# Kernel optimization log

Measured on AMD Instinct MI355X. Metric: run time of the kernel, lower is better.

The kernel has to match this reference:

```python
import jax, jax.numpy as jnp
import numpy as np

B, E, H, NY, NX = 16, 128, 4, 32, 32


def setup_inputs() -> dict:
    key = jax.random.key(0)
    ks = jax.random.split(key, 7)
    w = lambda k, shape: jax.random.normal(k, shape, jnp.float32) * 0.02
    return {
        "x": jax.random.normal(ks[0], (B, E, NY, NX), jnp.float32),
        "Wk": w(ks[1], (E, E)), "bk": jnp.zeros((E,), jnp.float32),
        "Wq": w(ks[2], (E, E)), "bq": jnp.zeros((E,), jnp.float32),
        "Wv": w(ks[3], (E, E)), "bv": jnp.zeros((E,), jnp.float32),
        "Wu": w(ks[4], (E, E)), "bu": jnp.zeros((E,), jnp.float32),
        "pos_enc": w(ks[5], (H, (2 * NY - 1) * (2 * NX - 1))),
    }


def _conv1x1(x, W, b):
    # 1x1 conv == channel-mixing linear: (B,C,y,x) -> (B,O,y,x)
    return jnp.einsum('bcyx,oc->boyx', x, W) + b[None, :, None, None]


def _rel_indices(ny, nx):
    y = jnp.arange(ny)
    x = jnp.arange(nx)
    y1, x1, y2, x2 = jnp.meshgrid(y, x, y, x, indexing='ij')
    idx = (y1 - y2 + ny - 1) * (2 * nx - 1) + (x1 - x2 + nx - 1)
    return idx.reshape(ny * nx, ny * nx)  # (N, N)


def reference(x, Wk, bk, Wq, bq, Wv, bv, Wu, bu, pos_enc):
    b, e, ny, nx = x.shape
    h = pos_enc.shape[0]
    hc = e // h
    n = ny * nx
    scale = hc ** (-0.5)

    keys = _conv1x1(x, Wk, bk).reshape(b, h, hc, n)
    queries = _conv1x1(x, Wq, bq).reshape(b, h, hc, n)
    values = _conv1x1(x, Wv, bv).reshape(b, h, hc, n)

    # att[b,h,k,q] = sum_c keys[b,h,c,k] * queries[b,h,c,q]
    att = jnp.einsum('bhck,bhcq->bhkq', keys, queries) * scale

    # gathered relative position bias: (H, N, N)
    idx = _rel_indices(ny, nx)
    rel = pos_enc[:, idx]
    att = att + rel[None]

    # softmax over the key axis (dim=-2), as in the original
    att = jax.nn.softmax(att, axis=-2)

    out = jnp.einsum('bhck,bhkq->bhcq', values, att).reshape(b, e, ny, nx)
    return _conv1x1(out, Wu, bu)
```

## Files before the change

kernel.cpp:

```cpp
#include <hip/hip_runtime.h>
#include <hip/hip_bf16.h>

#define BN 16
#define EN 128
#define HN 4
#define HCN 32
#define NN 1024
#define POSN 3969

typedef short short8 __attribute__((ext_vector_type(8)));
typedef float f32x4 __attribute__((ext_vector_type(4)));

#define MFMA16(a, b, c) __builtin_amdgcn_mfma_f32_16x16x32_bf16((a), (b), (c), 0, 0, 0)

union Frag {
  short8 s8;
  uint2 u2[2];
  unsigned int u[4];
  unsigned short us[8];
};

__device__ __forceinline__ unsigned short bfbits(float x) {
  union { __hip_bfloat16 h; unsigned short u; } c;
  c.h = __float2bfloat16(x);
  return c.u;
}

__device__ __forceinline__ unsigned int pk2(float lo, float hi) {
  union { __hip_bfloat162 h2; unsigned int u; } c;
  c.h2 = __float22bfloat162_rn(make_float2(lo, hi));
  return c.u;
}

__global__ __launch_bounds__(256) void prep_kernel(
    const float* __restrict__ pos,
    const float* __restrict__ Wk, const float* __restrict__ Wq,
    const float* __restrict__ Wv, const float* __restrict__ Wu,
    unsigned short* __restrict__ bias, Frag* __restrict__ wtab,
    Frag* __restrict__ whitab, Frag* __restrict__ wlotab)
{
  const int b0 = blockIdx.x, t = threadIdx.x;
  if (b0 < 189) {
    const int gid = b0 * 256 + t;
    const int l = gid & 63;
    const int t2 = gid >> 6;
    const int dxi = t2 % 3;
    const int dy31 = (t2 / 3) % 63;
    const int h = t2 / 189;
    const int rowk0 = (l >> 4) * 4, colq = l & 15;
    const float log2e = 1.4426950408889634f;
    unsigned int bits[4];
#pragma unroll
    for (int j = 0; j < 4; ++j) {
      const int dx = (dxi - 1) * 16 + rowk0 + j - colq + 31;
      bits[j] = (unsigned int)bfbits(pos[h * POSN + dy31 * 63 + dx] * log2e);
    }
    uint2 o;
    o.x = bits[0] | (bits[1] << 16);
    o.y = bits[2] | (bits[3] << 16);
    *(uint2*)(bias + (size_t)gid * 4) = o;
  } else if (b0 < 213) {
    const int fid = (b0 - 189) * 256 + t;
    const int z = fid >> 11, rem = fid & 2047;
    const int ot = rem >> 8, ks = (rem >> 6) & 3, l = rem & 63;
    const float* W = (z == 0) ? Wk : (z == 1) ? Wq : Wv;
    const int o = ot * 16 + (l & 15), lq = l >> 4;
    const float* wp = W + (size_t)o * EN + ks * 32 + lq * 4;
    float4 wa = *(const float4*)wp;
    float4 wb2 = *(const float4*)(wp + 16);
    Frag f;
    f.u[0] = pk2(wa.x, wa.y);   f.u[1] = pk2(wa.z, wa.w);
    f.u[2] = pk2(wb2.x, wb2.y); f.u[3] = pk2(wb2.z, wb2.w);
    wtab[fid] = f;
  } else {
    const int fid = (b0 - 213) * 256 + t;
    const int ot = fid >> 8, ks = (fid >> 6) & 3, l = fid & 63;
    const int o = ot * 16 + (l & 15), lq = l >> 4;
    const float* wp = Wu + (size_t)o * EN + ks * 32 + lq * 4;
    float4 wa = *(const float4*)wp;
    float4 wb2 = *(const float4*)(wp + 16);
    float v[8] = {wa.x, wa.y, wa.z, wa.w, wb2.x, wb2.y, wb2.z, wb2.w};
    unsigned short hb[8]; float lf[8];
#pragma unroll
    for (int e = 0; e < 8; ++e) {
      __hip_bfloat16 hh = __float2bfloat16(v[e]);
      union { __hip_bfloat16 h; unsigned short u; } c; c.h = hh;
      hb[e] = c.u;
      lf[e] = v[e] - __bfloat162float(hh);
    }
    Frag fh, fl;
#pragma unroll
    for (int e = 0; e < 4; ++e)
      fh.u[e] = hb[2 * e] | ((unsigned int)hb[2 * e + 1] << 16);
    fl.u[0] = pk2(lf[0], lf[1]); fl.u[1] = pk2(lf[2], lf[3]);
    fl.u[2] = pk2(lf[4], lf[5]); fl.u[3] = pk2(lf[6], lf[7]);
    whitab[fid] = fh;
    wlotab[fid] = fl;
  }
}

__global__ __launch_bounds__(256) void conv_qkv_mfma(
    const float* __restrict__ x, const Frag* __restrict__ wtab,
    const float* __restrict__ bk, __hip_bfloat16* __restrict__ kb,
    const float* __restrict__ bq, __hip_bfloat16* __restrict__ qb,
    const float* __restrict__ bv, __hip_bfloat16* __restrict__ vb)
{
  const int n0 = blockIdx.x * 32;
  const int bb = blockIdx.y;
  const int t = threadIdx.x, w = t >> 6, l = t & 63;
  const int l15 = l & 15, lq = l >> 4;

  __shared__ unsigned short xs[32][132];

  {
    const float* xb = x + (size_t)bb * EN * NN + n0;
    const int n = t & 31, cg = (t >> 5) * 4;
#pragma unroll
    for (int i = 0; i < 4; ++i) {
      const int cb = cg + i * 32;
      float a0 = xb[(size_t)(cb + 0) * NN + n];
      float a1 = xb[(size_t)(cb + 1) * NN + n];
      float a2 = xb[(size_t)(cb + 2) * NN + n];
      float a3 = xb[(size_t)(cb + 3) * NN + n];
      uint2 v; v.x = pk2(a0, a1); v.y = pk2(a2, a3);
      *(uint2*)&xs[n][cb] = v;
    }
  }
  __syncthreads();

#pragma unroll
  for (int z = 0; z < 3; ++z) {
    const float* bias = (z == 0) ? bk : (z == 1) ? bq : bv;
    __hip_bfloat16* out = (z == 0) ? kb : (z == 1) ? qb : vb;

    Frag wf[2][4];
#pragma unroll
    for (int r = 0; r < 2; ++r)
#pragma unroll
      for (int ks = 0; ks < 4; ++ks)
        wf[r][ks] = wtab[(((size_t)z * 8 + (w * 2 + r)) * 4 + ks) * 64 + l];

    f32x4 acc[2][2];
#pragma unroll
    for (int r = 0; r < 2; ++r)
#pragma unroll
      for (int nt = 0; nt < 2; ++nt) acc[r][nt] = 0.f;

#pragma unroll
    for (int ks = 0; ks < 4; ++ks) {
#pragma unroll
      for (int nt = 0; nt < 2; ++nt) {
        Frag xf;
        xf.u2[0] = *(const uint2*)&xs[nt * 16 + l15][ks * 32 + lq * 4];
        xf.u2[1] = *(const uint2*)&xs[nt * 16 + l15][ks * 32 + lq * 4 + 16];
        if (z < 2) {
          acc[0][nt] = MFMA16(wf[0][ks].s8, xf.s8, acc[0][nt]);
          acc[1][nt] = MFMA16(wf[1][ks].s8, xf.s8, acc[1][nt]);
        } else {
          acc[0][nt] = MFMA16(xf.s8, wf[0][ks].s8, acc[0][nt]);
          acc[1][nt] = MFMA16(xf.s8, wf[1][ks].s8, acc[1][nt]);
        }
      }
    }

    if (z < 2) {
#pragma unroll
      for (int r = 0; r < 2; ++r) {
        const int ob = (w * 2 + r) * 16 + lq * 4;
        const int hh = ob >> 5;
        const int pofs = hh * 32 + ((ob >> 2) & 3) * 8 + ((ob & 16) ? 4 : 0);
        float4 b4 = *(const float4*)(bias + ob);
#pragma unroll
        for (int nt = 0; nt < 2; ++nt) {
          const int n = n0 + nt * 16 + l15;
          f32x4 a = acc[r][nt];
          uint2 o2;
          o2.x = pk2(a[0] + b4.x, a[1] + b4.y);
          o2.y = pk2(a[2] + b4.z, a[3] + b4.w);
          *(uint2*)(out + (size_t)(bb * NN + n) * 128 + pofs) = o2;
        }
      }
    } else {
#pragma unroll
      for (int r = 0; r < 2; ++r) {
        const int o = (w * 2 + r) * 16 + l15;
        const int c = o & 31, hh = o >> 5;
        const float bsc = bias[o];
#pragma unroll
        for (int nt = 0; nt < 2; ++nt) {
          const int nb = n0 + nt * 16 + lq * 4;
          const int kbk = nb >> 5, k32 = nb & 31;
          const int pofs = ((k32 >> 2) & 3) * 8 + ((k32 & 16) ? 4 : 0);
          f32x4 a = acc[r][nt];
          uint2 o2;
          o2.x = pk2(a[0] + bsc, a[1] + bsc);
          o2.y = pk2(a[2] + bsc, a[3] + bsc);
          *(uint2*)(out + ((size_t)((bb * 4 + hh) * 32 + c) * 32 + kbk) * 32 + pofs) = o2;
        }
      }
    }
  }
}

__global__ __launch_bounds__(256, 4) void attn_mfma_kernel(
    const __hip_bfloat16* __restrict__ kp,
    const __hip_bfloat16* __restrict__ qp,
    const __hip_bfloat16* __restrict__ vp,
    const unsigned short* __restrict__ bias,
    __hip_bfloat16* __restrict__ Opb,
    float* __restrict__ lp)
{
  const int bx = blockIdx.x;
  const int qi = bx & 7, s = bx >> 3;
  const int h = blockIdx.y, b = blockIdx.z;
  const int t = threadIdx.x, w = t >> 6, l = t & 63;
  const int l15 = l & 15, lq = l >> 4;

  __shared__ Frag Kf[2][8][64];
  __shared__ Frag Vf[2][8][64];

  const __hip_bfloat16* kBase = kp + (size_t)b * 131072 + h * 32 + (size_t)l15 * 128 + lq * 8;
  const __hip_bfloat16* vBase = vp + (size_t)((b * 4 + h) * 32 + l15) * 1024 + lq * 8;
  const unsigned short* biasB = bias + (size_t)h * 48384 + l * 4;

#define KADDR(CHG, KT) ((const Frag*)(kBase + (size_t)((CHG) * 128 + (KT) * 16) * 128))
#define VADDR(CHG, SL) ((const Frag*)(vBase + (size_t)((SL) >> 2) * 16384 + ((CHG) * 4 + ((SL) & 3)) * 32))

  const int qt0 = qi * 8 + w * 2;
  Frag qf[2];
  qf[0] = *(const Frag*)(qp + (size_t)(b * 1024 + (qt0 + 0) * 16 + l15) * 128 + h * 32 + lq * 8);
  qf[1] = *(const Frag*)(qp + (size_t)(b * 1024 + (qt0 + 1) * 16 + l15) * 128 + h * 32 + lq * 8);
  const int qy[2] = {(qt0 + 0) >> 1, (qt0 + 1) >> 1};
  const int qx1[2] = {(qt0 + 0) & 1, (qt0 + 1) & 1};

  {
    const int chg = s * 4;
    Kf[0][w][l]     = *KADDR(chg, w);
    Kf[0][w + 4][l] = *KADDR(chg, w + 4);
    Vf[0][w][l]     = *VADDR(chg, w);
    Vf[0][w + 4][l] = *VADDR(chg, w + 4);
  }
  __syncthreads();

  f32x4 O[2][2];
#pragma unroll
  for (int mt = 0; mt < 2; ++mt)
#pragma unroll
    for (int nt = 0; nt < 2; ++nt) O[mt][nt] = 0.f;
  f32x4 Lacc[2]; Lacc[0] = 0.f; Lacc[1] = 0.f;

  Frag ones;
  ones.u[0] = 0x3F803F80u; ones.u[1] = 0x3F803F80u;
  ones.u[2] = 0x3F803F80u; ones.u[3] = 0x3F803F80u;

  const float SCALE2 = 0.17677669529663687f * 1.4426950408889634f;

  for (int c4 = 0; c4 < 4; ++c4) {
    const int buf = c4 & 1;
    const int chg = s * 4 + c4;

    Frag kn[2], vn[2];
    if (c4 < 3) {
      kn[0] = *KADDR(chg + 1, w);
      kn[1] = *KADDR(chg + 1, w + 4);
      vn[0] = *VADDR(chg + 1, w);
      vn[1] = *VADDR(chg + 1, w + 4);
    }

#pragma unroll
    for (int hh2 = 0; hh2 < 2; ++hh2) {
      short8 ka[4], va[4];
#pragma unroll
      for (int kt = 0; kt < 4; ++kt) ka[kt] = Kf[buf][hh2 * 4 + kt][l].s8;
#pragma unroll
      for (int mt = 0; mt < 2; ++mt)
#pragma unroll
        for (int kh = 0; kh < 2; ++kh)
          va[mt * 2 + kh] = Vf[buf][mt * 4 + hh2 * 2 + kh][l].s8;

#pragma unroll
      for (int nt = 0; nt < 2; ++nt) {
        uint2 bw[4];
#pragma unroll
        for (int kt = 0; kt < 4; ++kt) {
          const int ktg = chg * 8 + hh2 * 4 + kt;
          const int off = ((ktg >> 1) - qy[nt] + 31) * 768 + ((ktg & 1) - qx1[nt] + 1) * 256;
          bw[kt] = *(const uint2*)(biasB + off);
        }

        __builtin_amdgcn_s_setprio(1);
        f32x4 S[4];
#pragma unroll
        for (int kt = 0; kt < 4; ++kt) {
          f32x4 z = 0.f;
          S[kt] = MFMA16(ka[kt], qf[nt].s8, z);
        }
        __builtin_amdgcn_s_setprio(0);

        Frag B0, B1;
#pragma unroll
        for (int kt = 0; kt < 4; ++kt) {
          const float b0 = __uint_as_float(bw[kt].x << 16);
          const float b1 = __uint_as_float(bw[kt].x & 0xffff0000u);
          const float b2 = __uint_as_float(bw[kt].y << 16);
          const float b3 = __uint_as_float(bw[kt].y & 0xffff0000u);
          float p0 = exp2f(fmaf(S[kt][0], SCALE2, b0));
          float p1 = exp2f(fmaf(S[kt][1], SCALE2, b1));
          float p2 = exp2f(fmaf(S[kt][2], SCALE2, b2));
          float p3 = exp2f(fmaf(S[kt][3], SCALE2, b3));
          unsigned int lo = pk2(p0, p1), hi = pk2(p2, p3);
          if (kt < 2) { B0.u[kt * 2] = lo; B0.u[kt * 2 + 1] = hi; }
          else        { B1.u[(kt - 2) * 2] = lo; B1.u[(kt - 2) * 2 + 1] = hi; }
        }

        __builtin_amdgcn_s_setprio(1);
        O[0][nt] = MFMA16(va[0], B0.s8, O[0][nt]);
        O[0][nt] = MFMA16(va[1], B1.s8, O[0][nt]);
        O[1][nt] = MFMA16(va[2], B0.s8, O[1][nt]);
        O[1][nt] = MFMA16(va[3], B1.s8, O[1][nt]);
        Lacc[nt] = MFMA16(ones.s8, B0.s8, Lacc[nt]);
        Lacc[nt] = MFMA16(ones.s8, B1.s8, Lacc[nt]);
        __builtin_amdgcn_s_setprio(0);
      }
    }

    if (c4 < 3) {
      Kf[buf ^ 1][w][l]     = kn[0];
      Kf[buf ^ 1][w + 4][l] = kn[1];
      Vf[buf ^ 1][w][l]     = vn[0];
      Vf[buf ^ 1][w + 4][l] = vn[1];
      __syncthreads();
    }
  }
#undef KADDR
#undef VADDR

  if (lq == 0) {
#pragma unroll
    for (int nt = 0; nt < 2; ++nt)
      lp[((size_t)(s * 16 + b) * 4 + h) * 1024 + (qt0 + nt) * 16 + l15] = Lacc[nt][0];
  }

  __hip_bfloat16* obb = Opb + ((size_t)(s * 16 + b) * 1024) * 128 + h * 32 + lq * 8;
#pragma unroll
  for (int nt = 0; nt < 2; ++nt) {
    const int n = (qt0 + nt) * 16 + l15;
    Frag f;
    f.u[0] = pk2(O[0][nt][0], O[0][nt][1]);
    f.u[1] = pk2(O[0][nt][2], O[0][nt][3]);
    f.u[2] = pk2(O[1][nt][0], O[1][nt][1]);
    f.u[3] = pk2(O[1][nt][2], O[1][nt][3]);
    *(Frag*)(obb + (size_t)n * 128) = f;
  }
}

__global__ __launch_bounds__(256, 2) void conv_final_mfma(
    const __hip_bfloat16* __restrict__ Opb,
    const float* __restrict__ lp,
    const Frag* __restrict__ whitab, const Frag* __restrict__ wlotab,
    const float* __restrict__ bu, float* __restrict__ out)
{
  const int n0 = blockIdx.x * 32;
  const int bb = blockIdx.y;
  const int t = threadIdx.x, w = t >> 6, l = t & 63;
  const int l15 = l & 15, lq = l >> 4;

  __shared__ float rls[4][32];
  if (t < 128) {
    const int h = t >> 5, nl = t & 31;
    const float l0 = lp[((size_t)(0 * 16 + bb) * 4 + h) * 1024 + n0 + nl];
    const float l1 = lp[((size_t)(1 * 16 + bb) * 4 + h) * 1024 + n0 + nl];
    rls[h][nl] = 1.0f / (l0 + l1);
  }

  Frag whi[2][4], wlo[2][4];
#pragma unroll
  for (int r = 0; r < 2; ++r)
#pragma unroll
    for (int ks = 0; ks < 4; ++ks) {
      const int idx = (((w * 2 + r) * 4) + ks) * 64 + l;
      whi[r][ks] = whitab[idx];
      wlo[r][ks] = wlotab[idx];
    }
  __syncthreads();

  f32x4 acc[2][2];
#pragma unroll
  for (int r = 0; r < 2; ++r)
#pragma unroll
    for (int nt = 0; nt < 2; ++nt) acc[r][nt] = 0.f;

#pragma unroll
  for (int s = 0; s < 2; ++s) {
#pragma unroll
    for (int h = 0; h < 4; ++h) {
      Frag a2[2];
#pragma unroll
      for (int nt = 0; nt < 2; ++nt) {
        const int n = n0 + nt * 16 + l15;
        Frag af = *(const Frag*)(Opb + ((size_t)((s * 16 + bb) * 1024 + n)) * 128 + h * 32 + lq * 8);
        const float sc = rls[h][nt * 16 + l15];
        Frag as;
#pragma unroll
        for (int e = 0; e < 4; ++e) {
          const float f0 = __uint_as_float((unsigned int)af.us[2 * e] << 16) * sc;
          const float f1 = __uint_as_float((unsigned int)af.us[2 * e + 1] << 16) * sc;
          as.u[e] = pk2(f0, f1);
        }
        a2[nt] = as;
      }
#pragma unroll
      for (int r = 0; r < 2; ++r)
#pragma unroll
        for (int nt = 0; nt < 2; ++nt) {
          acc[r][nt] = MFMA16(a2[nt].s8, whi[r][h].s8, acc[r][nt]);
          acc[r][nt] = MFMA16(a2[nt].s8, wlo[r][h].s8, acc[r][nt]);
        }
    }
  }

#pragma unroll
  for (int r = 0; r < 2; ++r) {
    const int o = (w * 2 + r) * 16 + l15;
    const float bo = bu[o];
#pragma unroll
    for (int nt = 0; nt < 2; ++nt) {
      const int nb = n0 + nt * 16 + lq * 4;
      f32x4 a = acc[r][nt];
      float4 res = make_float4(a[0] + bo, a[1] + bo, a[2] + bo, a[3] + bo);
      *(float4*)(out + ((size_t)bb * EN + o) * NN + nb) = res;
    }
  }
}

extern "C" void kernel_launch(void* const* d_in, const int* in_sizes, int n_in,
                              void* d_out, int out_size, void* d_ws, size_t ws_size,
                              hipStream_t stream)
{
  const float* x   = (const float*)d_in[0];
  const float* Wk  = (const float*)d_in[1];
  const float* bk  = (const float*)d_in[2];
  const float* Wq  = (const float*)d_in[3];
  const float* bq  = (const float*)d_in[4];
  const float* Wv  = (const float*)d_in[5];
  const float* bv  = (const float*)d_in[6];
  const float* Wu  = (const float*)d_in[7];
  const float* bu  = (const float*)d_in[8];
  const float* pos = (const float*)d_in[9];

  char* ws = (char*)d_ws;
  __hip_bfloat16* kb = (__hip_bfloat16*)(ws);
  __hip_bfloat16* qb = (__hip_bfloat16*)(ws + (size_t)4194304);
  __hip_bfloat16* vb = (__hip_bfloat16*)(ws + (size_t)8388608);
  unsigned short* bias = (unsigned short*)(ws + (size_t)12582912);
  Frag* wtab   = (Frag*)(ws + (size_t)12969984);
  Frag* whitab = (Frag*)(ws + (size_t)13068288);
  Frag* wlotab = (Frag*)(ws + (size_t)13101056);
  float* lp = (float*)(ws + (size_t)13133824);
  __hip_bfloat16* Opb = (__hip_bfloat16*)(ws + (size_t)13658112);

  prep_kernel<<<221, 256, 0, stream>>>(pos, Wk, Wq, Wv, Wu, bias, wtab, whitab, wlotab);

  dim3 g1(32, BN);
  conv_qkv_mfma<<<g1, 256, 0, stream>>>(x, wtab, bk, kb, bq, qb, bv, vb);

  dim3 g2(16, HN, BN);
  attn_mfma_kernel<<<g2, 256, 0, stream>>>(kb, qb, vb, bias, Opb, lp);

  dim3 g3(32, BN);
  conv_final_mfma<<<g3, 256, 0, stream>>>(Opb, lp, whitab, wlotab, bu, (float*)d_out);
}
```

Before: 59.30 us.

## Merge prep and QKV conv kernels; use direct global-to-LDS loads in attention

Folds the prep kernel (bias table and Wu hi/lo split) into the QKV conv kernel as extra blocks. The conv blocks now read and convert Wk/Wq/Wv to bf16 fragments themselves, so the wtab table and one kernel launch go away. In attention, K/V double-buffer prefetch uses global_load_lds, which writes straight into LDS instead of going through registers. All bias loads for a chunk are also hoisted ahead of compute. In exchange, the conv blocks do redundant weight conversion, and register pressure from the hoisted bias array rises.

New measurement: 66.76 us. +12.6%, slower.

```diff
diff --git a/kernel.cpp b/kernel.cpp
--- a/kernel.cpp
+++ b/kernel.cpp
@@ -32,82 +32,73 @@
   return c.u;
 }
 
-__global__ __launch_bounds__(256) void prep_kernel(
-    const float* __restrict__ pos,
-    const float* __restrict__ Wk, const float* __restrict__ Wq,
-    const float* __restrict__ Wv, const float* __restrict__ Wu,
-    unsigned short* __restrict__ bias, Frag* __restrict__ wtab,
-    Frag* __restrict__ whitab, Frag* __restrict__ wlotab)
+__device__ __forceinline__ void load_lds16(const void* g, void* l) {
+  __builtin_amdgcn_global_load_lds(
+      (const __attribute__((address_space(1))) void*)g,
+      (__attribute__((address_space(3))) void*)l, 16, 0, 0);
+}
+
+__global__ __launch_bounds__(256) void qkv_prep_kernel(
+    const float* __restrict__ x,
+    const float* __restrict__ Wk, const float* __restrict__ bk, __hip_bfloat16* __restrict__ kb,
+    const float* __restrict__ Wq, const float* __restrict__ bq, __hip_bfloat16* __restrict__ qb,
+    const float* __restrict__ Wv, const float* __restrict__ bv, __hip_bfloat16* __restrict__ vb,
+    const float* __restrict__ Wu, const float* __restrict__ pos,
+    unsigned short* __restrict__ bias, Frag* __restrict__ whitab, Frag* __restrict__ wlotab)
 {
-  const int b0 = blockIdx.x, t = threadIdx.x;
-  if (b0 < 189) {
-    const int gid = b0 * 256 + t;
-    const int l = gid & 63;
-    const int t2 = gid >> 6;
-    const int dxi = t2 % 3;
-    const int dy31 = (t2 / 3) % 63;
-    const int h = t2 / 189;
-    const int rowk0 = (l >> 4) * 4, colq = l & 15;
-    const float log2e = 1.4426950408889634f;
-    unsigned int bits[4];
-#pragma unroll
-    for (int j = 0; j < 4; ++j) {
-      const int dx = (dxi - 1) * 16 + rowk0 + j - colq + 31;
-      bits[j] = (unsigned int)bfbits(pos[h * POSN + dy31 * 63 + dx] * log2e);
-    }
-    uint2 o;
-    o.x = bits[0] | (bits[1] << 16);
-    o.y = bits[2] | (bits[3] << 16);
-    *(uint2*)(bias + (size_t)gid * 4) = o;
-  } else if (b0 < 213) {
-    const int fid = (b0 - 189) * 256 + t;
-    const int z = fid >> 11, rem = fid & 2047;
-    const int ot = rem >> 8, ks = (rem >> 6) & 3, l = rem & 63;
-    const float* W = (z == 0) ? Wk : (z == 1) ? Wq : Wv;
-    const int o = ot * 16 + (l & 15), lq = l >> 4;
-    const float* wp = W + (size_t)o * EN + ks * 32 + lq * 4;
-    float4 wa = *(const float4*)wp;
-    float4 wb2 = *(const float4*)(wp + 16);
-    Frag f;
-    f.u[0] = pk2(wa.x, wa.y);   f.u[1] = pk2(wa.z, wa.w);
-    f.u[2] = pk2(wb2.x, wb2.y); f.u[3] = pk2(wb2.z, wb2.w);
-    wtab[fid] = f;
-  } else {
-    const int fid = (b0 - 213) * 256 + t;
-    const int ot = fid >> 8, ks = (fid >> 6) & 3, l = fid & 63;
-    const int o = ot * 16 + (l & 15), lq = l >> 4;
-    const float* wp = Wu + (size_t)o * EN + ks * 32 + lq * 4;
-    float4 wa = *(const float4*)wp;
-    float4 wb2 = *(const float4*)(wp + 16);
-    float v[8] = {wa.x, wa.y, wa.z, wa.w, wb2.x, wb2.y, wb2.z, wb2.w};
-    unsigned short hb[8]; float lf[8];
-#pragma unroll
-    for (int e = 0; e < 8; ++e) {
-      __hip_bfloat16 hh = __float2bfloat16(v[e]);
-      union { __hip_bfloat16 h; unsigned short u; } c; c.h = hh;
-      hb[e] = c.u;
-      lf[e] = v[e] - __bfloat162float(hh);
-    }
-    Frag fh, fl;
-#pragma unroll
-    for (int e = 0; e < 4; ++e)
-      fh.u[e] = hb[2 * e] | ((unsigned int)hb[2 * e + 1] << 16);
-    fl.u[0] = pk2(lf[0], lf[1]); fl.u[1] = pk2(lf[2], lf[3]);
-    fl.u[2] = pk2(lf[4], lf[5]); fl.u[3] = pk2(lf[6], lf[7]);
-    whitab[fid] = fh;
-    wlotab[fid] = fl;
-  }
-}
-
-__global__ __launch_bounds__(256) void conv_qkv_mfma(
-    const float* __restrict__ x, const Frag* __restrict__ wtab,
-    const float* __restrict__ bk, __hip_bfloat16* __restrict__ kb,
-    const float* __restrict__ bq, __hip_bfloat16* __restrict__ qb,
-    const float* __restrict__ bv, __hip_bfloat16* __restrict__ vb)
-{
-  const int n0 = blockIdx.x * 32;
-  const int bb = blockIdx.y;
-  const int t = threadIdx.x, w = t >> 6, l = t & 63;
+  const int bid = blockIdx.x, t = threadIdx.x;
+
+  if (bid >= 512) {
+    if (bid < 701) {
+      const int gid = (bid - 512) * 256 + t;
+      const int l = gid & 63;
+      const int t2 = gid >> 6;
+      const int dxi = t2 % 3;
+      const int dy31 = (t2 / 3) % 63;
+      const int h = t2 / 189;
+      const int rowk0 = (l >> 4) * 4, colq = l & 15;
+      const float log2e = 1.4426950408889634f;
+      unsigned int bits[4];
+#pragma unroll
+      for (int j = 0; j < 4; ++j) {
+        const int dx = (dxi - 1) * 16 + rowk0 + j - colq + 31;
+        bits[j] = (unsigned int)bfbits(pos[h * POSN + dy31 * 63 + dx] * log2e);
+      }
+      uint2 o;
+      o.x = bits[0] | (bits[1] << 16);
+      o.y = bits[2] | (bits[3] << 16);
+      *(uint2*)(bias + (size_t)gid * 4) = o;
+    } else {
+      const int fid = (bid - 701) * 256 + t;
+      const int ot = fid >> 8, ks = (fid >> 6) & 3, l = fid & 63;
+      const int o = ot * 16 + (l & 15), lq = l >> 4;
+      const float* wp = Wu + (size_t)o * EN + ks * 32 + lq * 4;
+      float4 wa = *(const float4*)wp;
+      float4 wb2 = *(const float4*)(wp + 16);
+      float v[8] = {wa.x, wa.y, wa.z, wa.w, wb2.x, wb2.y, wb2.z, wb2.w};
+      unsigned short hb[8]; float lf[8];
+#pragma unroll
+      for (int e = 0; e < 8; ++e) {
+        __hip_bfloat16 hh = __float2bfloat16(v[e]);
+        union { __hip_bfloat16 h; unsigned short u; } c; c.h = hh;
+        hb[e] = c.u;
+        lf[e] = v[e] - __bfloat162float(hh);
+      }
+      Frag fh, fl;
+#pragma unroll
+      for (int e = 0; e < 4; ++e)
+        fh.u[e] = hb[2 * e] | ((unsigned int)hb[2 * e + 1] << 16);
+      fl.u[0] = pk2(lf[0], lf[1]); fl.u[1] = pk2(lf[2], lf[3]);
+      fl.u[2] = pk2(lf[4], lf[5]); fl.u[3] = pk2(lf[6], lf[7]);
+      whitab[fid] = fh;
+      wlotab[fid] = fl;
+    }
+    return;
+  }
+
+  const int n0 = (bid & 31) * 32;
+  const int bb = bid >> 5;
+  const int w = t >> 6, l = t & 63;
   const int l15 = l & 15, lq = l >> 4;
 
   __shared__ unsigned short xs[32][132];
@@ -130,15 +121,25 @@
 
 #pragma unroll
   for (int z = 0; z < 3; ++z) {
-    const float* bias = (z == 0) ? bk : (z == 1) ? bq : bv;
+    const float* W = (z == 0) ? Wk : (z == 1) ? Wq : Wv;
+    const float* bias_v = (z == 0) ? bk : (z == 1) ? bq : bv;
     __hip_bfloat16* out = (z == 0) ? kb : (z == 1) ? qb : vb;
 
     Frag wf[2][4];
 #pragma unroll
-    for (int r = 0; r < 2; ++r)
-#pragma unroll
-      for (int ks = 0; ks < 4; ++ks)
-        wf[r][ks] = wtab[(((size_t)z * 8 + (w * 2 + r)) * 4 + ks) * 64 + l];
+    for (int r = 0; r < 2; ++r) {
+      const int o = (w * 2 + r) * 16 + l15;
+#pragma unroll
+      for (int ks = 0; ks < 4; ++ks) {
+        const float* wp = W + (size_t)o * EN + ks * 32 + lq * 4;
+        float4 wa = *(const float4*)wp;
+        float4 wb2 = *(const float4*)(wp + 16);
+        Frag f;
+        f.u[0] = pk2(wa.x, wa.y);   f.u[1] = pk2(wa.z, wa.w);
+        f.u[2] = pk2(wb2.x, wb2.y); f.u[3] = pk2(wb2.z, wb2.w);
+        wf[r][ks] = f;
+      }
+    }
 
     f32x4 acc[2][2];
 #pragma unroll
@@ -169,7 +170,7 @@
         const int ob = (w * 2 + r) * 16 + lq * 4;
         const int hh = ob >> 5;
         const int pofs = hh * 32 + ((ob >> 2) & 3) * 8 + ((ob & 16) ? 4 : 0);
-        float4 b4 = *(const float4*)(bias + ob);
+        float4 b4 = *(const float4*)(bias_v + ob);
 #pragma unroll
         for (int nt = 0; nt < 2; ++nt) {
           const int n = n0 + nt * 16 + l15;
@@ -185,7 +186,7 @@
       for (int r = 0; r < 2; ++r) {
         const int o = (w * 2 + r) * 16 + l15;
         const int c = o & 31, hh = o >> 5;
-        const float bsc = bias[o];
+        const float bsc = bias_v[o];
 #pragma unroll
         for (int nt = 0; nt < 2; ++nt) {
           const int nb = n0 + nt * 16 + lq * 4;
@@ -235,10 +236,10 @@
 
   {
     const int chg = s * 4;
-    Kf[0][w][l]     = *KADDR(chg, w);
-    Kf[0][w + 4][l] = *KADDR(chg, w + 4);
-    Vf[0][w][l]     = *VADDR(chg, w);
-    Vf[0][w + 4][l] = *VADDR(chg, w + 4);
+    load_lds16(KADDR(chg, w),     &Kf[0][w][0]);
+    load_lds16(KADDR(chg, w + 4), &Kf[0][w + 4][0]);
+    load_lds16(VADDR(chg, w),     &Vf[0][w][0]);
+    load_lds16(VADDR(chg, w + 4), &Vf[0][w + 4][0]);
   }
   __syncthreads();
 
@@ -259,35 +260,38 @@
     const int buf = c4 & 1;
     const int chg = s * 4 + c4;
 
-    Frag kn[2], vn[2];
     if (c4 < 3) {
-      kn[0] = *KADDR(chg + 1, w);
-      kn[1] = *KADDR(chg + 1, w + 4);
-      vn[0] = *VADDR(chg + 1, w);
-      vn[1] = *VADDR(chg + 1, w + 4);
-    }
-
-#pragma unroll
-    for (int hh2 = 0; hh2 < 2; ++hh2) {
-      short8 ka[4], va[4];
-#pragma unroll
-      for (int kt = 0; kt < 4; ++kt) ka[kt] = Kf[buf][hh2 * 4 + kt][l].s8;
-#pragma unroll
-      for (int mt = 0; mt < 2; ++mt)
-#pragma unroll
-        for (int kh = 0; kh < 2; ++kh)
-          va[mt * 2 + kh] = Vf[buf][mt * 4 + hh2 * 2 + kh][l].s8;
-
-#pragma unroll
-      for (int nt = 0; nt < 2; ++nt) {
-        uint2 bw[4];
+      load_lds16(KADDR(chg + 1, w),     &Kf[buf ^ 1][w][0]);
+      load_lds16(KADDR(chg + 1, w + 4), &Kf[buf ^ 1][w + 4][0]);
+      load_lds16(VADDR(chg + 1, w),     &Vf[buf ^ 1][w][0]);
+      load_lds16(VADDR(chg + 1, w + 4), &Vf[buf ^ 1][w + 4][0]);
+    }
+
+    uint2 bw[2][2][4];
+#pragma unroll
+    for (int hh2 = 0; hh2 < 2; ++hh2)
+#pragma unroll
+      for (int nt = 0; nt < 2; ++nt)
 #pragma unroll
         for (int kt = 0; kt < 4; ++kt) {
           const int ktg = chg * 8 + hh2 * 4 + kt;
           const int off = ((ktg >> 1) - qy[nt] + 31) * 768 + ((ktg & 1) - qx1[nt] + 1) * 256;
-          bw[kt] = *(const uint2*)(biasB + off);
-        }
-
+          bw[hh2][nt][kt] = *(const uint2*)(biasB + off);
+        }
+
+#pragma unroll
+    for (int hh2 = 0; hh2 < 2; ++hh2) {
+      short8 ka[4], va[4];
+#pragma unroll
+      for (int kt = 0; kt < 4; ++kt) ka[kt] = Kf[buf][hh2 * 4 + kt][l].s8;
+#pragma unroll
+      for (int mt = 0; mt < 2; ++mt)
+#pragma unroll
+        for (int kh = 0; kh < 2; ++kh)
+          va[mt * 2 + kh] = Vf[buf][mt * 4 + hh2 * 2 + kh][l].s8;
+
+#pragma unroll
+      for (int nt = 0; nt < 2; ++nt) {
         __builtin_amdgcn_s_setprio(1);
         f32x4 S[4];
 #pragma unroll
@@ -300,10 +304,10 @@
         Frag B0, B1;
 #pragma unroll
         for (int kt = 0; kt < 4; ++kt) {
-          const float b0 = __uint_as_float(bw[kt].x << 16);
-          const float b1 = __uint_as_float(bw[kt].x & 0xffff0000u);
-          const float b2 = __uint_as_float(bw[kt].y << 16);
-          const float b3 = __uint_as_float(bw[kt].y & 0xffff0000u);
+          const float b0 = __uint_as_float(bw[hh2][nt][kt].x << 16);
+          const float b1 = __uint_as_float(bw[hh2][nt][kt].x & 0xffff0000u);
+          const float b2 = __uint_as_float(bw[hh2][nt][kt].y << 16);
+          const float b3 = __uint_as_float(bw[hh2][nt][kt].y & 0xffff0000u);
           float p0 = exp2f(fmaf(S[kt][0], SCALE2, b0));
           float p1 = exp2f(fmaf(S[kt][1], SCALE2, b1));
           float p2 = exp2f(fmaf(S[kt][2], SCALE2, b2));
@@ -324,13 +328,7 @@
       }
     }
 
-    if (c4 < 3) {
-      Kf[buf ^ 1][w][l]     = kn[0];
-      Kf[buf ^ 1][w + 4][l] = kn[1];
-      Vf[buf ^ 1][w][l]     = vn[0];
-      Vf[buf ^ 1][w + 4][l] = vn[1];
-      __syncthreads();
-    }
+    if (c4 < 3) __syncthreads();
   }
 #undef KADDR
 #undef VADDR
@@ -453,16 +451,13 @@
   __hip_bfloat16* qb = (__hip_bfloat16*)(ws + (size_t)4194304);
   __hip_bfloat16* vb = (__hip_bfloat16*)(ws + (size_t)8388608);
   unsigned short* bias = (unsigned short*)(ws + (size_t)12582912);
-  Frag* wtab   = (Frag*)(ws + (size_t)12969984);
   Frag* whitab = (Frag*)(ws + (size_t)13068288);
   Frag* wlotab = (Frag*)(ws + (size_t)13101056);
   float* lp = (float*)(ws + (size_t)13133824);
   __hip_bfloat16* Opb = (__hip_bfloat16*)(ws + (size_t)13658112);
 
-  prep_kernel<<<221, 256, 0, stream>>>(pos, Wk, Wq, Wv, Wu, bias, wtab, whitab, wlotab);
-
-  dim3 g1(32, BN);
-  conv_qkv_mfma<<<g1, 256, 0, stream>>>(x, wtab, bk, kb, bq, qb, bv, vb);
+  qkv_prep_kernel<<<709, 256, 0, stream>>>(x, Wk, bk, kb, Wq, bq, qb, Wv, bv, vb,
+                                           Wu, pos, bias, whitab, wlotab);
 
   dim3 g2(16, HN, BN);
   attn_mfma_kernel<<<g2, 256, 0, stream>>>(kb, qb, vb, bias, Opb, lp);
```
